# Optimization experiments

Hardware: AMD Instinct MI355X
Metric: run time of the kernel (lower is better)

Reference implementation:

```python
import jax, jax.numpy as jnp
import numpy as np

N_NODES = 50000
N_EDGES = 800000


def setup_inputs() -> dict:
    key = jax.random.key(0)
    ks = jax.random.split(key, 12)
    x = jax.random.normal(ks[0], (N_NODES, 500), dtype=jnp.float32)
    edge_src = jax.random.randint(ks[1], (N_EDGES,), 0, N_NODES, dtype=jnp.int32)
    edge_dst = jax.random.randint(ks[2], (N_EDGES,), 0, N_NODES, dtype=jnp.int32)
    edge_vals = jax.random.uniform(ks[3], (N_EDGES,), dtype=jnp.float32) * 0.1
    def w(k, fan_in, fan_out):
        s = 1.0 / np.sqrt(fan_in)
        return jax.random.uniform(k, (fan_in, fan_out), dtype=jnp.float32, minval=-s, maxval=s)
    W1 = w(ks[4], 500, 128)
    b1 = jnp.zeros((128,), jnp.float32)
    W2 = w(ks[5], 128, 64)
    b2 = jnp.zeros((64,), jnp.float32)
    W3 = w(ks[6], 64, 16)
    b3 = jnp.zeros((16,), jnp.float32)
    We = w(ks[7], 64, 64)
    be = jnp.zeros((64,), jnp.float32)
    return {"x": x, "edge_vals": edge_vals, "W1": W1, "b1": b1, "W2": W2,
            "b2": b2, "W3": W3, "b3": b3, "We": We, "be": be,
            "edge_src": edge_src, "edge_dst": edge_dst}


def reference(x, edge_vals, W1, b1, W2, b2, W3, b3, We, be, edge_src, edge_dst):
    n = x.shape[0]

    def gcn_layer(h, W, b):
        # GraphConvolution: support = h @ W ; out = spmm(adj, support) + b
        support = h @ W                                   # [N, d_out]
        msg = support[edge_dst] * edge_vals[:, None]      # [E, d_out]
        agg = jax.ops.segment_sum(msg, edge_src, num_segments=n)
        return agg + b

    h = jax.nn.relu(gcn_layer(x, W1, b1))
    # dropout omitted (eval mode, training=False)
    h = jax.nn.relu(gcn_layer(h, W2, b2))
    out1 = jax.nn.log_softmax(gcn_layer(h, W3, b3), axis=1)
    out2 = h @ We + be
    return (out1, out2)
```

## Files before the change

kernel.cpp:

```cpp
#include <hip/hip_runtime.h>
#include <hip/hip_bf16.h>
#include <math.h>

#define N_NODES 50000
#define N_EDGES 800000

typedef __attribute__((ext_vector_type(8))) short bf16x8;
typedef __attribute__((ext_vector_type(4))) float f32x4;

__device__ inline unsigned short f2bf(float f) {
    unsigned u = __float_as_uint(f);
    unsigned r = (u + 0x7fffu + ((u >> 16) & 1u)) >> 16;
    return (unsigned short)r;
}

__device__ inline bf16x8 pack8(float4 a0, float4 a1) {
    union { __hip_bfloat162 h2[4]; bf16x8 v; } u;
    u.h2[0] = __float22bfloat162_rn(make_float2(a0.x, a0.y));
    u.h2[1] = __float22bfloat162_rn(make_float2(a0.z, a0.w));
    u.h2[2] = __float22bfloat162_rn(make_float2(a1.x, a1.y));
    u.h2[3] = __float22bfloat162_rn(make_float2(a1.z, a1.w));
    return u.v;
}

__global__ __launch_bounds__(256) void convert_weights_kernel(
    const float* __restrict__ W1, const float* __restrict__ W2,
    const float* __restrict__ We, const float* __restrict__ W3,
    unsigned short* __restrict__ W1frag, unsigned short* __restrict__ W2bf,
    unsigned short* __restrict__ Wcat)
{
    int t = blockIdx.x * 256 + threadIdx.x;
    if (t < 65536) {
        int h = t >> 15;
        int r1 = t & 32767;
        int j = r1 >> 13;
        int r2 = r1 & 8191;
        int s = r2 >> 9;
        int r3 = r2 & 511;
        int lane = r3 >> 3, jj = r3 & 7;
        int k = s * 32 + (lane >> 4) * 8 + jj;
        int n = h * 64 + j * 16 + (lane & 15);
        float v = (k < 500) ? W1[k * 128 + n] : 0.0f;
        W1frag[t] = f2bf(v);
    } else if (t < 65536 + 8192) {
        int t2 = t - 65536;
        int n = t2 >> 7, k = t2 & 127;
        W2bf[t2] = f2bf(W2[k * 64 + n]);
    } else if (t < 65536 + 8192 + 5120) {
        int t3 = t - 65536 - 8192;
        int n = t3 >> 6, k = t3 & 63;
        float v = (n < 64) ? We[k * 64 + n] : W3[k * 16 + (n - 64)];
        Wcat[t3] = f2bf(v);
    }
}

__global__ __launch_bounds__(256, 2) void gemm1_mfma_kernel(
    const float* __restrict__ A,
    const unsigned short* __restrict__ W1frag,
    unsigned short* __restrict__ C)
{
    __shared__ __align__(16) unsigned short Bs[32768];

    const int t = threadIdx.x;
    const int h  = blockIdx.x & 1;
    const int br = blockIdx.x >> 1;
    const int lane = t & 63;
    const int wave = t >> 6;
    const int r = lane & 15, q = lane >> 4;

    {
        const uint4* src = reinterpret_cast<const uint4*>(W1frag + h * 32768);
        uint4* dst = reinterpret_cast<uint4*>(Bs);
#pragma unroll
        for (int i = 0; i < 16; ++i)
            dst[t + i * 256] = src[t + i * 256];
    }
    __syncthreads();

    const int col0 = h * 64;

    for (int c = br * 4 + wave; c < 3125; c += 1024) {
        const float* ap = A + (size_t)(c * 16 + r) * 500;

        f32x4 acc[4];
#pragma unroll
        for (int j = 0; j < 4; ++j) acc[j] = {0.f, 0.f, 0.f, 0.f};

#pragma unroll 4
        for (int s = 0; s < 16; ++s) {
            const int kb = s * 32 + q * 8;
            const int k0 = kb < 496 ? kb : 496;
            const int k1 = (kb + 4) < 496 ? (kb + 4) : 496;
            float4 a0 = *reinterpret_cast<const float4*>(ap + k0);
            float4 a1 = *reinterpret_cast<const float4*>(ap + k1);
            bf16x8 af = pack8(a0, a1);
#pragma unroll
            for (int j = 0; j < 4; ++j) {
                bf16x8 b = *reinterpret_cast<const bf16x8*>(
                    &Bs[(size_t)((j * 16 + s) * 64 + lane) * 8]);
                acc[j] = __builtin_amdgcn_mfma_f32_16x16x32_bf16(af, b, acc[j], 0, 0, 0);
            }
        }

#pragma unroll
        for (int reg = 0; reg < 4; ++reg) {
            const int grow = c * 16 + q * 4 + reg;
#pragma unroll
            for (int j = 0; j < 4; ++j)
                C[(size_t)grow * 128 + col0 + j * 16 + r] = f2bf(acc[j][reg]);
        }
    }
}

__global__ __launch_bounds__(256) void gemm2_mfma_kernel(
    const unsigned short* __restrict__ A,
    const unsigned short* __restrict__ Bt,
    unsigned short* __restrict__ C)
{
    const int wid  = (blockIdx.x * 256 + threadIdx.x) >> 6;
    const int lane = threadIdx.x & 63;
    const int r = lane & 15, q = lane >> 4;
    const int row0 = wid * 16;
    const int arow = row0 + r;
    const bool valid = arow < N_NODES;
    const unsigned short* ap = A + (size_t)arow * 128 + q * 8;

    const f32x4 zero = {0.0f, 0.0f, 0.0f, 0.0f};
    f32x4 acc[4];
#pragma unroll
    for (int j = 0; j < 4; ++j) acc[j] = zero;

#pragma unroll
    for (int s = 0; s < 4; ++s) {
        bf16x8 af = {};
        if (valid) af = *reinterpret_cast<const bf16x8*>(ap + s * 32);
#pragma unroll
        for (int j = 0; j < 4; ++j) {
            bf16x8 bfr = *reinterpret_cast<const bf16x8*>(
                Bt + (size_t)(j * 16 + r) * 128 + s * 32 + q * 8);
            acc[j] = __builtin_amdgcn_mfma_f32_16x16x32_bf16(af, bfr, acc[j], 0, 0, 0);
        }
    }

#pragma unroll
    for (int reg = 0; reg < 4; ++reg) {
        int grow = row0 + q * 4 + reg;
        if (grow < N_NODES) {
#pragma unroll
            for (int j = 0; j < 4; ++j)
                C[(size_t)grow * 64 + j * 16 + r] = f2bf(acc[j][reg]);
        }
    }
}

__global__ __launch_bounds__(256) void gemm3_mfma_kernel(
    const unsigned short* __restrict__ A,
    const unsigned short* __restrict__ Bt,
    const float* __restrict__ be,
    float* __restrict__ out2,
    float* __restrict__ sup3)
{
    const int wid  = (blockIdx.x * 256 + threadIdx.x) >> 6;
    const int lane = threadIdx.x & 63;
    const int r = lane & 15, q = lane >> 4;
    const int row0 = wid * 16;
    const int arow = row0 + r;
    const bool valid = arow < N_NODES;
    const unsigned short* ap = A + (size_t)arow * 64 + q * 8;

    const f32x4 zero = {0.0f, 0.0f, 0.0f, 0.0f};
    f32x4 acc[5];
#pragma unroll
    for (int j = 0; j < 5; ++j) acc[j] = zero;

#pragma unroll
    for (int s = 0; s < 2; ++s) {
        bf16x8 af = {};
        if (valid) af = *reinterpret_cast<const bf16x8*>(ap + s * 32);
#pragma unroll
        for (int j = 0; j < 5; ++j) {
            bf16x8 bfr = *reinterpret_cast<const bf16x8*>(
                Bt + (size_t)(j * 16 + r) * 64 + s * 32 + q * 8);
            acc[j] = __builtin_amdgcn_mfma_f32_16x16x32_bf16(af, bfr, acc[j], 0, 0, 0);
        }
    }

    float bev[4];
#pragma unroll
    for (int j = 0; j < 4; ++j) bev[j] = be[j * 16 + r];

#pragma unroll
    for (int reg = 0; reg < 4; ++reg) {
        int grow = row0 + q * 4 + reg;
        if (grow < N_NODES) {
#pragma unroll
            for (int j = 0; j < 4; ++j)
                out2[(size_t)grow * 64 + j * 16 + r] = acc[j][reg] + bev[j];
            sup3[(size_t)grow * 16 + r] = acc[4][reg];
        }
    }
}

__global__ __launch_bounds__(256) void hist_kernel(
    const int* __restrict__ src, int* __restrict__ counts)
{
    int e = blockIdx.x * 256 + threadIdx.x;
    if (e < N_EDGES) atomicAdd(&counts[src[e]], 1);
}

__global__ __launch_bounds__(1024) void scan_kernel(
    const int* __restrict__ counts, int* __restrict__ row_ptr,
    int* __restrict__ cursor)
{
    constexpr int Q = N_NODES / 4;
    const int t = threadIdx.x;
    const int lane = t & 63, wave = t >> 6;
    __shared__ int wsum[16];
    __shared__ int carry_s;
    int carry = 0;
    const int4* c4 = reinterpret_cast<const int4*>(counts);
    int4* rp4 = reinterpret_cast<int4*>(row_ptr);
    int4* cu4 = reinterpret_cast<int4*>(cursor);

    for (int base = 0; base < Q; base += 1024) {
        const int g = base + t;
        int4 v = {0, 0, 0, 0};
        if (g < Q) v = c4[g];
        const int s = v.x + v.y + v.z + v.w;

        int incl = s;
#pragma unroll
        for (int off = 1; off < 64; off <<= 1) {
            int n = __shfl_up(incl, off, 64);
            if (lane >= off) incl += n;
        }
        if (lane == 63) wsum[wave] = incl;
        __syncthreads();
        if (t < 16) {
            int w = wsum[t];
            int inc = w;
#pragma unroll
            for (int off = 1; off < 16; off <<= 1) {
                int n = __shfl_up(inc, off, 64);
                if (t >= off) inc += n;
            }
            wsum[t] = inc - w;
            if (t == 15) carry_s = inc;
        }
        __syncthreads();
        if (g < Q) {
            int e0 = carry + wsum[wave] + (incl - s);
            int4 r;
            r.x = e0;
            r.y = r.x + v.x;
            r.z = r.y + v.y;
            r.w = r.z + v.z;
            rp4[g] = r;
            cu4[g] = r;
        }
        carry += carry_s;
        __syncthreads();
    }
    if (t == 0) row_ptr[N_NODES] = carry;
}

__global__ __launch_bounds__(256) void fill_kernel(
    const int* __restrict__ src, const int* __restrict__ dst,
    const float* __restrict__ vals, int* __restrict__ cursor,
    int2* __restrict__ pairs)
{
    int e = blockIdx.x * 256 + threadIdx.x;
    if (e >= N_EDGES) return;
    int pos = atomicAdd(&cursor[src[e]], 1);
    pairs[pos] = make_int2(dst[e], __float_as_int(vals[e]));
}

__global__ __launch_bounds__(256) void gather128_bf16_kernel(
    const unsigned short* __restrict__ support, const int2* __restrict__ pairs,
    const int* __restrict__ row_ptr, const float* __restrict__ b1,
    unsigned short* __restrict__ h1)
{
    const int node = blockIdx.x * 16 + (threadIdx.x >> 4);
    if (node >= N_NODES) return;
    const int lane = threadIdx.x & 15;
    int i = row_ptr[node];
    const int end = row_ptr[node + 1];

    float acc[8] = {};
    for (; i + 2 <= end; i += 2) {
        int2 p0 = pairs[i], p1 = pairs[i + 1];
        float v0 = __int_as_float(p0.y), v1 = __int_as_float(p1.y);
        uint4 r0 = *reinterpret_cast<const uint4*>(
            support + (size_t)p0.x * 128 + lane * 8);
        uint4 r1 = *reinterpret_cast<const uint4*>(
            support + (size_t)p1.x * 128 + lane * 8);
        unsigned w0[4] = {r0.x, r0.y, r0.z, r0.w};
        unsigned w1[4] = {r1.x, r1.y, r1.z, r1.w};
#pragma unroll
        for (int j = 0; j < 4; ++j) {
            acc[2 * j]     += __uint_as_float(w0[j] << 16) * v0;
            acc[2 * j + 1] += __uint_as_float(w0[j] & 0xffff0000u) * v0;
            acc[2 * j]     += __uint_as_float(w1[j] << 16) * v1;
            acc[2 * j + 1] += __uint_as_float(w1[j] & 0xffff0000u) * v1;
        }
    }
    if (i < end) {
        int2 p = pairs[i];
        float v = __int_as_float(p.y);
        uint4 r = *reinterpret_cast<const uint4*>(
            support + (size_t)p.x * 128 + lane * 8);
        unsigned w[4] = {r.x, r.y, r.z, r.w};
#pragma unroll
        for (int j = 0; j < 4; ++j) {
            acc[2 * j]     += __uint_as_float(w[j] << 16) * v;
            acc[2 * j + 1] += __uint_as_float(w[j] & 0xffff0000u) * v;
        }
    }
    const float4 ba = *reinterpret_cast<const float4*>(b1 + lane * 8);
    const float4 bb = *reinterpret_cast<const float4*>(b1 + lane * 8 + 4);
    float bias[8] = {ba.x, ba.y, ba.z, ba.w, bb.x, bb.y, bb.z, bb.w};
    unsigned short h[8];
#pragma unroll
    for (int j = 0; j < 8; ++j) {
        float v = acc[j] + bias[j];
        h[j] = f2bf(v > 0.0f ? v : 0.0f);
    }
    *reinterpret_cast<uint4*>(h1 + (size_t)node * 128 + lane * 8) =
        *reinterpret_cast<uint4*>(h);
}

__global__ __launch_bounds__(256) void gather64_bf16_kernel(
    const unsigned short* __restrict__ support, const int2* __restrict__ pairs,
    const int* __restrict__ row_ptr, const float* __restrict__ b2,
    unsigned short* __restrict__ h2)
{
    const int node = blockIdx.x * 32 + (threadIdx.x >> 3);
    if (node >= N_NODES) return;
    const int lane = threadIdx.x & 7;
    int i = row_ptr[node];
    const int end = row_ptr[node + 1];

    float acc[8] = {};
    for (; i + 2 <= end; i += 2) {
        int2 p0 = pairs[i], p1 = pairs[i + 1];
        float v0 = __int_as_float(p0.y), v1 = __int_as_float(p1.y);
        uint4 r0 = *reinterpret_cast<const uint4*>(
            support + (size_t)p0.x * 64 + lane * 8);
        uint4 r1 = *reinterpret_cast<const uint4*>(
            support + (size_t)p1.x * 64 + lane * 8);
        unsigned w0[4] = {r0.x, r0.y, r0.z, r0.w};
        unsigned w1[4] = {r1.x, r1.y, r1.z, r1.w};
#pragma unroll
        for (int j = 0; j < 4; ++j) {
            acc[2 * j]     += __uint_as_float(w0[j] << 16) * v0;
            acc[2 * j + 1] += __uint_as_float(w0[j] & 0xffff0000u) * v0;
            acc[2 * j]     += __uint_as_float(w1[j] << 16) * v1;
            acc[2 * j + 1] += __uint_as_float(w1[j] & 0xffff0000u) * v1;
        }
    }
    if (i < end) {
        int2 p = pairs[i];
        float v = __int_as_float(p.y);
        uint4 r = *reinterpret_cast<const uint4*>(
            support + (size_t)p.x * 64 + lane * 8);
        unsigned w[4] = {r.x, r.y, r.z, r.w};
#pragma unroll
        for (int j = 0; j < 4; ++j) {
            acc[2 * j]     += __uint_as_float(w[j] << 16) * v;
            acc[2 * j + 1] += __uint_as_float(w[j] & 0xffff0000u) * v;
        }
    }
    const float4 ba = *reinterpret_cast<const float4*>(b2 + lane * 8);
    const float4 bb = *reinterpret_cast<const float4*>(b2 + lane * 8 + 4);
    float bias[8] = {ba.x, ba.y, ba.z, ba.w, bb.x, bb.y, bb.z, bb.w};
    unsigned short h[8];
#pragma unroll
    for (int j = 0; j < 8; ++j) {
        float v = acc[j] + bias[j];
        h[j] = f2bf(v > 0.0f ? v : 0.0f);
    }
    *reinterpret_cast<uint4*>(h2 + (size_t)node * 64 + lane * 8) =
        *reinterpret_cast<uint4*>(h);
}

__global__ __launch_bounds__(256) void gather16_kernel(
    const float* __restrict__ support, const int2* __restrict__ pairs,
    const int* __restrict__ row_ptr, float* __restrict__ agg)
{
    const int node = blockIdx.x * 64 + (threadIdx.x >> 2);
    if (node >= N_NODES) return;
    const int lane = threadIdx.x & 3;
    int i = row_ptr[node];
    const int end = row_ptr[node + 1];

    float4 acc0 = {0, 0, 0, 0};
    float4 acc1 = {0, 0, 0, 0};

    for (; i + 2 <= end; i += 2) {
        int2 p0 = pairs[i];
        int2 p1 = pairs[i + 1];
        float v0 = __int_as_float(p0.y);
        float v1 = __int_as_float(p1.y);
        const float4 m0 = *reinterpret_cast<const float4*>(
            support + (size_t)p0.x * 16 + lane * 4);
        const float4 m1 = *reinterpret_cast<const float4*>(
            support + (size_t)p1.x * 16 + lane * 4);
        acc0.x += m0.x * v0; acc0.y += m0.y * v0;
        acc0.z += m0.z * v0; acc0.w += m0.w * v0;
        acc1.x += m1.x * v1; acc1.y += m1.y * v1;
        acc1.z += m1.z * v1; acc1.w += m1.w * v1;
    }
    if (i < end) {
        int2 p = pairs[i];
        float v = __int_as_float(p.y);
        const float4 m = *reinterpret_cast<const float4*>(
            support + (size_t)p.x * 16 + lane * 4);
        acc0.x += m.x * v; acc0.y += m.y * v;
        acc0.z += m.z * v; acc0.w += m.w * v;
    }
    acc0.x += acc1.x; acc0.y += acc1.y; acc0.z += acc1.z; acc0.w += acc1.w;
    *reinterpret_cast<float4*>(agg + (size_t)node * 16 + lane * 4) = acc0;
}

__global__ __launch_bounds__(256) void logsoftmax_kernel(
    const float* __restrict__ agg, const float* __restrict__ b3,
    float* __restrict__ out)
{
    int row = blockIdx.x * 256 + threadIdx.x;
    if (row >= N_NODES) return;
    float v[16];
    const float4* p = reinterpret_cast<const float4*>(agg + (size_t)row * 16);
#pragma unroll
    for (int i = 0; i < 4; ++i) {
        float4 q = p[i];
        v[i * 4 + 0] = q.x + b3[i * 4 + 0];
        v[i * 4 + 1] = q.y + b3[i * 4 + 1];
        v[i * 4 + 2] = q.z + b3[i * 4 + 2];
        v[i * 4 + 3] = q.w + b3[i * 4 + 3];
    }
    float mx = v[0];
#pragma unroll
    for (int i = 1; i < 16; ++i) mx = fmaxf(mx, v[i]);
    float s = 0.0f;
#pragma unroll
    for (int i = 0; i < 16; ++i) s += expf(v[i] - mx);
    float lse = mx + logf(s);
    float4* o = reinterpret_cast<float4*>(out + (size_t)row * 16);
#pragma unroll
    for (int i = 0; i < 4; ++i)
        o[i] = make_float4(v[i * 4 + 0] - lse, v[i * 4 + 1] - lse,
                           v[i * 4 + 2] - lse, v[i * 4 + 3] - lse);
}

extern "C" void kernel_launch(void* const* d_in, const int* in_sizes, int n_in,
                              void* d_out, int out_size, void* d_ws, size_t ws_size,
                              hipStream_t stream)
{
    const float* x         = (const float*)d_in[0];
    const float* edge_vals = (const float*)d_in[1];
    const float* W1 = (const float*)d_in[2];
    const float* b1 = (const float*)d_in[3];
    const float* W2 = (const float*)d_in[4];
    const float* b2 = (const float*)d_in[5];
    const float* W3 = (const float*)d_in[6];
    const float* b3 = (const float*)d_in[7];
    const float* We = (const float*)d_in[8];
    const float* be = (const float*)d_in[9];
    const int* esrc = (const int*)d_in[10];
    const int* edst = (const int*)d_in[11];

    float* out1 = (float*)d_out;
    float* out2 = (float*)d_out + (size_t)N_NODES * 16;

    char* ws = (char*)d_ws;
    float* bufA    = (float*)(ws);
    float* bufB    = (float*)(ws + 25600000);
    float* bufC    = (float*)(ws + 51200000);
    int*   counts  = (int*)  (ws + 54400000);
    int*   row_ptr = (int*)  (ws + 54600064);
    int*   cursor  = (int*)  (ws + 54800128);
    int2*  pairs   = (int2*) (ws + 55000192);

    unsigned short* W1frag = (unsigned short*)bufC;
    unsigned short* W2bf = (unsigned short*)((char*)bufC + 131072);
    unsigned short* Wcat = (unsigned short*)((char*)bufC + 147456);

    unsigned short* sup1bf = (unsigned short*)bufA;
    unsigned short* h1bf   = (unsigned short*)bufB;
    unsigned short* sup2bf = (unsigned short*)bufA;
    unsigned short* h2bf   = (unsigned short*)bufB;
    float*          sup3   = bufA;
    float*          agg3   = bufC;

    const int WB = (N_NODES / 16 + 3) / 4;
    const int EB = (N_EDGES + 255) / 256;

    convert_weights_kernel<<<308, 256, 0, stream>>>(W1, W2, We, W3, W1frag, W2bf, Wcat);
    hipMemsetAsync(counts, 0, (size_t)N_NODES * 4, stream);
    hist_kernel<<<EB, 256, 0, stream>>>(esrc, counts);
    scan_kernel<<<1, 1024, 0, stream>>>(counts, row_ptr, cursor);
    fill_kernel<<<EB, 256, 0, stream>>>(esrc, edst, edge_vals, cursor, pairs);

    gemm1_mfma_kernel<<<512, 256, 0, stream>>>(x, W1frag, sup1bf);

    gather128_bf16_kernel<<<(N_NODES + 15) / 16, 256, 0, stream>>>(
        sup1bf, pairs, row_ptr, b1, h1bf);

    gemm2_mfma_kernel<<<WB, 256, 0, stream>>>(h1bf, W2bf, sup2bf);

    gather64_bf16_kernel<<<(N_NODES + 31) / 32, 256, 0, stream>>>(
        sup2bf, pairs, row_ptr, b2, h2bf);

    gemm3_mfma_kernel<<<WB, 256, 0, stream>>>(h2bf, Wcat, be, out2, sup3);

    gather16_kernel<<<(N_NODES + 63) / 64, 256, 0, stream>>>(
        sup3, pairs, row_ptr, agg3);

    logsoftmax_kernel<<<(N_NODES + 255) / 256, 256, 0, stream>>>(agg3, b3, out1);
}
```

Baseline: 371.1 us.

## Fuse weight conversion with histogram, fuse gather16 with log-softmax, widen gathers

Merges the weight-conversion and edge-histogram kernels into one launch and fuses the layer-3 gather with log-softmax, which removes the intermediate agg buffer and two launches. The gather kernels now give each node a full wavefront that splits its edges across lane groups and combines them with xor shuffles, to get more memory-level parallelism per node. The small GEMMs load pre-fragmented weights into LDS instead of reading strided global memory. Risks: more threads sit idle on low-degree nodes, and the shuffle reductions add work.

```diff
diff --git a/kernel.cpp b/kernel.cpp
--- a/kernel.cpp
+++ b/kernel.cpp
@@ -23,189 +23,49 @@
     return u.v;
 }
 
-__global__ __launch_bounds__(256) void convert_weights_kernel(
+__global__ __launch_bounds__(256) void convert_hist_kernel(
     const float* __restrict__ W1, const float* __restrict__ W2,
     const float* __restrict__ We, const float* __restrict__ W3,
-    unsigned short* __restrict__ W1frag, unsigned short* __restrict__ W2bf,
-    unsigned short* __restrict__ Wcat)
-{
-    int t = blockIdx.x * 256 + threadIdx.x;
-    if (t < 65536) {
-        int h = t >> 15;
-        int r1 = t & 32767;
-        int j = r1 >> 13;
-        int r2 = r1 & 8191;
-        int s = r2 >> 9;
-        int r3 = r2 & 511;
-        int lane = r3 >> 3, jj = r3 & 7;
-        int k = s * 32 + (lane >> 4) * 8 + jj;
-        int n = h * 64 + j * 16 + (lane & 15);
-        float v = (k < 500) ? W1[k * 128 + n] : 0.0f;
-        W1frag[t] = f2bf(v);
-    } else if (t < 65536 + 8192) {
-        int t2 = t - 65536;
-        int n = t2 >> 7, k = t2 & 127;
-        W2bf[t2] = f2bf(W2[k * 64 + n]);
-    } else if (t < 65536 + 8192 + 5120) {
-        int t3 = t - 65536 - 8192;
-        int n = t3 >> 6, k = t3 & 63;
-        float v = (n < 64) ? We[k * 64 + n] : W3[k * 16 + (n - 64)];
-        Wcat[t3] = f2bf(v);
-    }
-}
-
-__global__ __launch_bounds__(256, 2) void gemm1_mfma_kernel(
-    const float* __restrict__ A,
-    const unsigned short* __restrict__ W1frag,
-    unsigned short* __restrict__ C)
-{
-    __shared__ __align__(16) unsigned short Bs[32768];
-
-    const int t = threadIdx.x;
-    const int h  = blockIdx.x & 1;
-    const int br = blockIdx.x >> 1;
-    const int lane = t & 63;
-    const int wave = t >> 6;
-    const int r = lane & 15, q = lane >> 4;
-
-    {
-        const uint4* src = reinterpret_cast<const uint4*>(W1frag + h * 32768);
-        uint4* dst = reinterpret_cast<uint4*>(Bs);
-#pragma unroll
-        for (int i = 0; i < 16; ++i)
-            dst[t + i * 256] = src[t + i * 256];
-    }
-    __syncthreads();
-
-    const int col0 = h * 64;
-
-    for (int c = br * 4 + wave; c < 3125; c += 1024) {
-        const float* ap = A + (size_t)(c * 16 + r) * 500;
-
-        f32x4 acc[4];
-#pragma unroll
-        for (int j = 0; j < 4; ++j) acc[j] = {0.f, 0.f, 0.f, 0.f};
-
-#pragma unroll 4
-        for (int s = 0; s < 16; ++s) {
-            const int kb = s * 32 + q * 8;
-            const int k0 = kb < 496 ? kb : 496;
-            const int k1 = (kb + 4) < 496 ? (kb + 4) : 496;
-            float4 a0 = *reinterpret_cast<const float4*>(ap + k0);
-            float4 a1 = *reinterpret_cast<const float4*>(ap + k1);
-            bf16x8 af = pack8(a0, a1);
-#pragma unroll
-            for (int j = 0; j < 4; ++j) {
-                bf16x8 b = *reinterpret_cast<const bf16x8*>(
-                    &Bs[(size_t)((j * 16 + s) * 64 + lane) * 8]);
-                acc[j] = __builtin_amdgcn_mfma_f32_16x16x32_bf16(af, b, acc[j], 0, 0, 0);
-            }
-        }
-
-#pragma unroll
-        for (int reg = 0; reg < 4; ++reg) {
-            const int grow = c * 16 + q * 4 + reg;
-#pragma unroll
-            for (int j = 0; j < 4; ++j)
-                C[(size_t)grow * 128 + col0 + j * 16 + r] = f2bf(acc[j][reg]);
-        }
-    }
-}
-
-__global__ __launch_bounds__(256) void gemm2_mfma_kernel(
-    const unsigned short* __restrict__ A,
-    const unsigned short* __restrict__ Bt,
-    unsigned short* __restrict__ C)
-{
-    const int wid  = (blockIdx.x * 256 + threadIdx.x) >> 6;
-    const int lane = threadIdx.x & 63;
-    const int r = lane & 15, q = lane >> 4;
-    const int row0 = wid * 16;
-    const int arow = row0 + r;
-    const bool valid = arow < N_NODES;
-    const unsigned short* ap = A + (size_t)arow * 128 + q * 8;
-
-    const f32x4 zero = {0.0f, 0.0f, 0.0f, 0.0f};
-    f32x4 acc[4];
-#pragma unroll
-    for (int j = 0; j < 4; ++j) acc[j] = zero;
-
-#pragma unroll
-    for (int s = 0; s < 4; ++s) {
-        bf16x8 af = {};
-        if (valid) af = *reinterpret_cast<const bf16x8*>(ap + s * 32);
-#pragma unroll
-        for (int j = 0; j < 4; ++j) {
-            bf16x8 bfr = *reinterpret_cast<const bf16x8*>(
-                Bt + (size_t)(j * 16 + r) * 128 + s * 32 + q * 8);
-            acc[j] = __builtin_amdgcn_mfma_f32_16x16x32_bf16(af, bfr, acc[j], 0, 0, 0);
-        }
-    }
-
-#pragma unroll
-    for (int reg = 0; reg < 4; ++reg) {
-        int grow = row0 + q * 4 + reg;
-        if (grow < N_NODES) {
-#pragma unroll
-            for (int j = 0; j < 4; ++j)
-                C[(size_t)grow * 64 + j * 16 + r] = f2bf(acc[j][reg]);
-        }
-    }
-}
-
-__global__ __launch_bounds__(256) void gemm3_mfma_kernel(
-    const unsigned short* __restrict__ A,
-    const unsigned short* __restrict__ Bt,
-    const float* __restrict__ be,
-    float* __restrict__ out2,
-    float* __restrict__ sup3)
-{
-    const int wid  = (blockIdx.x * 256 + threadIdx.x) >> 6;
-    const int lane = threadIdx.x & 63;
-    const int r = lane & 15, q = lane >> 4;
-    const int row0 = wid * 16;
-    const int arow = row0 + r;
-    const bool valid = arow < N_NODES;
-    const unsigned short* ap = A + (size_t)arow * 64 + q * 8;
-
-    const f32x4 zero = {0.0f, 0.0f, 0.0f, 0.0f};
-    f32x4 acc[5];
-#pragma unroll
-    for (int j = 0; j < 5; ++j) acc[j] = zero;
-
-#pragma unroll
-    for (int s = 0; s < 2; ++s) {
-        bf16x8 af = {};
-        if (valid) af = *reinterpret_cast<const bf16x8*>(ap + s * 32);
-#pragma unroll
-        for (int j = 0; j < 5; ++j) {
-            bf16x8 bfr = *reinterpret_cast<const bf16x8*>(
-                Bt + (size_t)(j * 16 + r) * 64 + s * 32 + q * 8);
-            acc[j] = __builtin_amdgcn_mfma_f32_16x16x32_bf16(af, bfr, acc[j], 0, 0, 0);
-        }
-    }
-
-    float bev[4];
-#pragma unroll
-    for (int j = 0; j < 4; ++j) bev[j] = be[j * 16 + r];
-
-#pragma unroll
-    for (int reg = 0; reg < 4; ++reg) {
-        int grow = row0 + q * 4 + reg;
-        if (grow < N_NODES) {
-#pragma unroll
-            for (int j = 0; j < 4; ++j)
-                out2[(size_t)grow * 64 + j * 16 + r] = acc[j][reg] + bev[j];
-            sup3[(size_t)grow * 16 + r] = acc[4][reg];
-        }
-    }
-}
-
-__global__ __launch_bounds__(256) void hist_kernel(
+    unsigned short* __restrict__ W1frag, unsigned short* __restrict__ W2frag,
+    unsigned short* __restrict__ Wcfrag,
     const int* __restrict__ src, int* __restrict__ counts)
 {
-    int e = blockIdx.x * 256 + threadIdx.x;
-    if (e < N_EDGES) atomicAdd(&counts[src[e]], 1);
+    if (blockIdx.x < 308) {
+        int t = blockIdx.x * 256 + threadIdx.x;
+        if (t < 65536) {
+            int h = t >> 15;
+            int r1 = t & 32767;
+            int j = r1 >> 13;
+            int r2 = r1 & 8191;
+            int s = r2 >> 9;
+            int r3 = r2 & 511;
+            int lane = r3 >> 3, jj = r3 & 7;
+            int k = s * 32 + (lane >> 4) * 8 + jj;
+            int n = h * 64 + j * 16 + (lane & 15);
+            float v = (k < 500) ? W1[k * 128 + n] : 0.0f;
+            W1frag[t] = f2bf(v);
+        } else if (t < 73728) {
+            int t2 = t - 65536;
+            int j = t2 >> 11;
+            int s = (t2 >> 9) & 3;
+            int lane = (t2 >> 3) & 63, jj = t2 & 7;
+            int k = s * 32 + (lane >> 4) * 8 + jj;
+            int n = j * 16 + (lane & 15);
+            W2frag[t2] = f2bf(W2[k * 64 + n]);
+        } else {
+            int t3 = t - 73728;
+            int j = t3 >> 10;
+            int s = (t3 >> 9) & 1;
+            int lane = (t3 >> 3) & 63, jj = t3 & 7;
+            int k = s * 32 + (lane >> 4) * 8 + jj;
+            int n = j * 16 + (lane & 15);
+            float v = (n < 64) ? We[k * 64 + n] : W3[k * 16 + (n - 64)];
+            Wcfrag[t3] = f2bf(v);
+        }
+    } else {
+        int e = (blockIdx.x - 308) * 256 + threadIdx.x;
+        if (e < N_EDGES) atomicAdd(&counts[src[e]], 1);
+    }
 }
 
 __global__ __launch_bounds__(1024) void scan_kernel(
@@ -275,25 +135,185 @@
     pairs[pos] = make_int2(dst[e], __float_as_int(vals[e]));
 }
 
-__global__ __launch_bounds__(256) void gather128_bf16_kernel(
+__global__ __launch_bounds__(256, 2) void gemm1_mfma_kernel(
+    const float* __restrict__ A,
+    const unsigned short* __restrict__ W1frag,
+    unsigned short* __restrict__ C)
+{
+    __shared__ __align__(16) unsigned short Bs[32768];
+
+    const int t = threadIdx.x;
+    const int h  = blockIdx.x & 1;
+    const int br = blockIdx.x >> 1;
+    const int lane = t & 63;
+    const int wave = t >> 6;
+    const int r = lane & 15, q = lane >> 4;
+
+    {
+        const uint4* src = reinterpret_cast<const uint4*>(W1frag + h * 32768);
+        uint4* dst = reinterpret_cast<uint4*>(Bs);
+#pragma unroll
+        for (int i = 0; i < 16; ++i)
+            dst[t + i * 256] = src[t + i * 256];
+    }
+    __syncthreads();
+
+    const int col0 = h * 64;
+
+    for (int c = br * 4 + wave; c < 3125; c += 1024) {
+        const float* ap = A + (size_t)(c * 16 + r) * 500;
+
+        f32x4 acc[4];
+#pragma unroll
+        for (int j = 0; j < 4; ++j) acc[j] = {0.f, 0.f, 0.f, 0.f};
+
+#pragma unroll 4
+        for (int s = 0; s < 16; ++s) {
+            const int kb = s * 32 + q * 8;
+            const int k0 = kb < 496 ? kb : 496;
+            const int k1 = (kb + 4) < 496 ? (kb + 4) : 496;
+            float4 a0 = *reinterpret_cast<const float4*>(ap + k0);
+            float4 a1 = *reinterpret_cast<const float4*>(ap + k1);
+            bf16x8 af = pack8(a0, a1);
+#pragma unroll
+            for (int j = 0; j < 4; ++j) {
+                bf16x8 b = *reinterpret_cast<const bf16x8*>(
+                    &Bs[(size_t)((j * 16 + s) * 64 + lane) * 8]);
+                acc[j] = __builtin_amdgcn_mfma_f32_16x16x32_bf16(af, b, acc[j], 0, 0, 0);
+            }
+        }
+
+#pragma unroll
+        for (int reg = 0; reg < 4; ++reg) {
+            const int grow = c * 16 + q * 4 + reg;
+#pragma unroll
+            for (int j = 0; j < 4; ++j)
+                C[(size_t)grow * 128 + col0 + j * 16 + r] = f2bf(acc[j][reg]);
+        }
+    }
+}
+
+__global__ __launch_bounds__(256) void gemm2_mfma_kernel(
+    const unsigned short* __restrict__ A,
+    const unsigned short* __restrict__ W2frag,
+    unsigned short* __restrict__ C)
+{
+    __shared__ __align__(16) unsigned short Bs[8192];
+
+    const int t = threadIdx.x;
+    const int lane = t & 63, wave = t >> 6;
+    const int r = lane & 15, q = lane >> 4;
+
+    {
+        const uint4* src = reinterpret_cast<const uint4*>(W2frag);
+        uint4* dst = reinterpret_cast<uint4*>(Bs);
+#pragma unroll
+        for (int i = 0; i < 4; ++i)
+            dst[t + i * 256] = src[t + i * 256];
+    }
+    __syncthreads();
+
+    const int c = blockIdx.x * 4 + wave;
+    if (c >= 3125) return;
+    const unsigned short* ap = A + (size_t)(c * 16 + r) * 128 + q * 8;
+
+    f32x4 acc[4];
+#pragma unroll
+    for (int j = 0; j < 4; ++j) acc[j] = {0.f, 0.f, 0.f, 0.f};
+
+#pragma unroll
+    for (int s = 0; s < 4; ++s) {
+        bf16x8 af = *reinterpret_cast<const bf16x8*>(ap + s * 32);
+#pragma unroll
+        for (int j = 0; j < 4; ++j) {
+            bf16x8 b = *reinterpret_cast<const bf16x8*>(
+                &Bs[(size_t)((j * 4 + s) * 64 + lane) * 8]);
+            acc[j] = __builtin_amdgcn_mfma_f32_16x16x32_bf16(af, b, acc[j], 0, 0, 0);
+        }
+    }
+
+#pragma unroll
+    for (int reg = 0; reg < 4; ++reg) {
+        const int grow = c * 16 + q * 4 + reg;
+#pragma unroll
+        for (int j = 0; j < 4; ++j)
+            C[(size_t)grow * 64 + j * 16 + r] = f2bf(acc[j][reg]);
+    }
+}
+
+__global__ __launch_bounds__(256) void gemm3_mfma_kernel(
+    const unsigned short* __restrict__ A,
+    const unsigned short* __restrict__ Wcfrag,
+    const float* __restrict__ be,
+    float* __restrict__ out2,
+    float* __restrict__ sup3)
+{
+    __shared__ __align__(16) unsigned short Bs[5120];
+
+    const int t = threadIdx.x;
+    const int lane = t & 63, wave = t >> 6;
+    const int r = lane & 15, q = lane >> 4;
+
+    {
+        const uint4* src = reinterpret_cast<const uint4*>(Wcfrag);
+        uint4* dst = reinterpret_cast<uint4*>(Bs);
+#pragma unroll
+        for (int i = 0; i < 2; ++i)
+            dst[t + i * 256] = src[t + i * 256];
+        if (t < 128) dst[512 + t] = src[512 + t];
+    }
+    __syncthreads();
+
+    const int c = blockIdx.x * 4 + wave;
+    if (c >= 3125) return;
+    const unsigned short* ap = A + (size_t)(c * 16 + r) * 64 + q * 8;
+
+    f32x4 acc[5];
+#pragma unroll
+    for (int j = 0; j < 5; ++j) acc[j] = {0.f, 0.f, 0.f, 0.f};
+
+#pragma unroll
+    for (int s = 0; s < 2; ++s) {
+        bf16x8 af = *reinterpret_cast<const bf16x8*>(ap + s * 32);
+#pragma unroll
+        for (int j = 0; j < 5; ++j) {
+            bf16x8 b = *reinterpret_cast<const bf16x8*>(
+                &Bs[(size_t)((j * 2 + s) * 64 + lane) * 8]);
+            acc[j] = __builtin_amdgcn_mfma_f32_16x16x32_bf16(af, b, acc[j], 0, 0, 0);
+        }
+    }
+
+    float bev[4];
+#pragma unroll
+    for (int j = 0; j < 4; ++j) bev[j] = be[j * 16 + r];
+
+#pragma unroll
+    for (int reg = 0; reg < 4; ++reg) {
+        const int grow = c * 16 + q * 4 + reg;
+#pragma unroll
+        for (int j = 0; j < 4; ++j)
+            out2[(size_t)grow * 64 + j * 16 + r] = acc[j][reg] + bev[j];
+        sup3[(size_t)grow * 16 + r] = acc[4][reg];
+    }
+}
+
+__global__ __launch_bounds__(256) void gather128_kernel(
     const unsigned short* __restrict__ support, const int2* __restrict__ pairs,
     const int* __restrict__ row_ptr, const float* __restrict__ b1,
     unsigned short* __restrict__ h1)
 {
-    const int node = blockIdx.x * 16 + (threadIdx.x >> 4);
-    if (node >= N_NODES) return;
-    const int lane = threadIdx.x & 15;
-    int i = row_ptr[node];
+    const int node = blockIdx.x * 4 + (threadIdx.x >> 6);
+    const int lane = threadIdx.x & 63;
+    const int f = lane & 15, e = lane >> 4;
+    int i = row_ptr[node] + e;
     const int end = row_ptr[node + 1];
 
     float acc[8] = {};
-    for (; i + 2 <= end; i += 2) {
-        int2 p0 = pairs[i], p1 = pairs[i + 1];
+    for (; i + 4 < end; i += 8) {
+        int2 p0 = pairs[i], p1 = pairs[i + 4];
         float v0 = __int_as_float(p0.y), v1 = __int_as_float(p1.y);
-        uint4 r0 = *reinterpret_cast<const uint4*>(
-            support + (size_t)p0.x * 128 + lane * 8);
-        uint4 r1 = *reinterpret_cast<const uint4*>(
-            support + (size_t)p1.x * 128 + lane * 8);
+        uint4 r0 = *reinterpret_cast<const uint4*>(support + (size_t)p0.x * 128 + f * 8);
+        uint4 r1 = *reinterpret_cast<const uint4*>(support + (size_t)p1.x * 128 + f * 8);
         unsigned w0[4] = {r0.x, r0.y, r0.z, r0.w};
         unsigned w1[4] = {r1.x, r1.y, r1.z, r1.w};
 #pragma unroll
@@ -307,8 +327,7 @@
     if (i < end) {
         int2 p = pairs[i];
         float v = __int_as_float(p.y);
-        uint4 r = *reinterpret_cast<const uint4*>(
-            support + (size_t)p.x * 128 + lane * 8);
+        uint4 r = *reinterpret_cast<const uint4*>(support + (size_t)p.x * 128 + f * 8);
         unsigned w[4] = {r.x, r.y, r.z, r.w};
 #pragma unroll
         for (int j = 0; j < 4; ++j) {
@@ -316,38 +335,43 @@
             acc[2 * j + 1] += __uint_as_float(w[j] & 0xffff0000u) * v;
         }
     }
-    const float4 ba = *reinterpret_cast<const float4*>(b1 + lane * 8);
-    const float4 bb = *reinterpret_cast<const float4*>(b1 + lane * 8 + 4);
-    float bias[8] = {ba.x, ba.y, ba.z, ba.w, bb.x, bb.y, bb.z, bb.w};
-    unsigned short h[8];
 #pragma unroll
     for (int j = 0; j < 8; ++j) {
-        float v = acc[j] + bias[j];
-        h[j] = f2bf(v > 0.0f ? v : 0.0f);
-    }
-    *reinterpret_cast<uint4*>(h1 + (size_t)node * 128 + lane * 8) =
-        *reinterpret_cast<uint4*>(h);
-}
-
-__global__ __launch_bounds__(256) void gather64_bf16_kernel(
+        acc[j] += __shfl_xor(acc[j], 16, 64);
+        acc[j] += __shfl_xor(acc[j], 32, 64);
+    }
+    if (e == 0) {
+        const float4 ba = *reinterpret_cast<const float4*>(b1 + f * 8);
+        const float4 bb = *reinterpret_cast<const float4*>(b1 + f * 8 + 4);
+        float bias[8] = {ba.x, ba.y, ba.z, ba.w, bb.x, bb.y, bb.z, bb.w};
+        unsigned short h[8];
+#pragma unroll
+        for (int j = 0; j < 8; ++j) {
+            float v = acc[j] + bias[j];
+            h[j] = f2bf(v > 0.0f ? v : 0.0f);
+        }
+        *reinterpret_cast<uint4*>(h1 + (size_t)node * 128 + f * 8) =
+            *reinterpret_cast<uint4*>(h);
+    }
+}
+
+__global__ __launch_bounds__(256) void gather64_kernel(
     const unsigned short* __restrict__ support, const int2* __restrict__ pairs,
     const int* __restrict__ row_ptr, const float* __restrict__ b2,
     unsigned short* __restrict__ h2)
 {
-    const int node = blockIdx.x * 32 + (threadIdx.x >> 3);
-    if (node >= N_NODES) return;
-    const int lane = threadIdx.x & 7;
-    int i = row_ptr[node];
+    const int node = blockIdx.x * 4 + (threadIdx.x >> 6);
+    const int lane = threadIdx.x & 63;
+    const int f = lane & 7, e = lane >> 3;
+    int i = row_ptr[node] + e;
     const int end = row_ptr[node + 1];
 
     float acc[8] = {};
-    for (; i + 2 <= end; i += 2) {
-        int2 p0 = pairs[i], p1 = pairs[i + 1];
+    for (; i + 8 < end; i += 16) {
+        int2 p0 = pairs[i], p1 = pairs[i + 8];
         float v0 = __int_as_float(p0.y), v1 = __int_as_float(p1.y);
-        uint4 r0 = *reinterpret_cast<const uint4*>(
-            support + (size_t)p0.x * 64 + lane * 8);
-        uint4 r1 = *reinterpret_cast<const uint4*>(
-            support + (size_t)p1.x * 64 + lane * 8);
+        uint4 r0 = *reinterpret_cast<const uint4*>(support + (size_t)p0.x * 64 + f * 8);
+        uint4 r1 = *reinterpret_cast<const uint4*>(support + (size_t)p1.x * 64 + f * 8);
         unsigned w0[4] = {r0.x, r0.y, r0.z, r0.w};
         unsigned w1[4] = {r1.x, r1.y, r1.z, r1.w};
 #pragma unroll
@@ -361,8 +385,7 @@
     if (i < end) {
         int2 p = pairs[i];
         float v = __int_as_float(p.y);
-        uint4 r = *reinterpret_cast<const uint4*>(
-            support + (size_t)p.x * 64 + lane * 8);
+        uint4 r = *reinterpret_cast<const uint4*>(support + (size_t)p.x * 64 + f * 8);
         unsigned w[4] = {r.x, r.y, r.z, r.w};
 #pragma unroll
         for (int j = 0; j < 4; ++j) {
@@ -370,86 +393,75 @@
             acc[2 * j + 1] += __uint_as_float(w[j] & 0xffff0000u) * v;
         }
     }
-    const float4 ba = *reinterpret_cast<const float4*>(b2 + lane * 8);
-    const float4 bb = *reinterpret_cast<const float4*>(b2 + lane * 8 + 4);
-    float bias[8] = {ba.x, ba.y, ba.z, ba.w, bb.x, bb.y, bb.z, bb.w};
-    unsigned short h[8];
 #pragma unroll
     for (int j = 0; j < 8; ++j) {
-        float v = acc[j] + bias[j];
-        h[j] = f2bf(v > 0.0f ? v : 0.0f);
-    }
-    *reinterpret_cast<uint4*>(h2 + (size_t)node * 64 + lane * 8) =
-        *reinterpret_cast<uint4*>(h);
-}
-
-__global__ __launch_bounds__(256) void gather16_kernel(
-    const float* __restrict__ support, const int2* __restrict__ pairs,
-    const int* __restrict__ row_ptr, float* __restrict__ agg)
-{
-    const int node = blockIdx.x * 64 + (threadIdx.x >> 2);
-    if (node >= N_NODES) return;
-    const int lane = threadIdx.x & 3;
-    int i = row_ptr[node];
+        acc[j] += __shfl_xor(acc[j], 8, 64);
+        acc[j] += __shfl_xor(acc[j], 16, 64);
+        acc[j] += __shfl_xor(acc[j], 32, 64);
+    }
+    if (e == 0) {
+        const float4 ba = *reinterpret_cast<const float4*>(b2 + f * 8);
+        const float4 bb = *reinterpret_cast<const float4*>(b2 + f * 8 + 4);
+        float bias[8] = {ba.x, ba.y, ba.z, ba.w, bb.x, bb.y, bb.z, bb.w};
+        unsigned short h[8];
+#pragma unroll
+        for (int j = 0; j < 8; ++j) {
+            float v = acc[j] + bias[j];
+            h[j] = f2bf(v > 0.0f ? v : 0.0f);
+        }
+        *reinterpret_cast<uint4*>(h2 + (size_t)node * 64 + f * 8) =
+            *reinterpret_cast<uint4*>(h);
+    }
+}
+
+__global__ __launch_bounds__(256) void gather16_lsm_kernel(
+    const float* __restrict__ sup3, const int2* __restrict__ pairs,
+    const int* __restrict__ row_ptr, const float* __restrict__ b3,
+    float* __restrict__ out1)
+{
+    const int node = blockIdx.x * 4 + (threadIdx.x >> 6);
+    const int lane = threadIdx.x & 63;
+    const int f = lane & 3, e = lane >> 2;
+    int i = row_ptr[node] + e;
     const int end = row_ptr[node + 1];
 
-    float4 acc0 = {0, 0, 0, 0};
-    float4 acc1 = {0, 0, 0, 0};
-
-    for (; i + 2 <= end; i += 2) {
-        int2 p0 = pairs[i];
-        int2 p1 = pairs[i + 1];
-        float v0 = __int_as_float(p0.y);
-        float v1 = __int_as_float(p1.y);
-        const float4 m0 = *reinterpret_cast<const float4*>(
-            support + (size_t)p0.x * 16 + lane * 4);
-        const float4 m1 = *reinterpret_cast<const float4*>(
-            support + (size_t)p1.x * 16 + lane * 4);
-        acc0.x += m0.x * v0; acc0.y += m0.y * v0;
-        acc0.z += m0.z * v0; acc0.w += m0.w * v0;
-        acc1.x += m1.x * v1; acc1.y += m1.y * v1;
-        acc1.z += m1.z * v1; acc1.w += m1.w * v1;
+    float4 acc = {0, 0, 0, 0};
+    for (; i + 16 < end; i += 32) {
+        int2 p0 = pairs[i], p1 = pairs[i + 16];
+        float v0 = __int_as_float(p0.y), v1 = __int_as_float(p1.y);
+        float4 m0 = *reinterpret_cast<const float4*>(sup3 + (size_t)p0.x * 16 + f * 4);
+        float4 m1 = *reinterpret_cast<const float4*>(sup3 + (size_t)p1.x * 16 + f * 4);
+        acc.x += m0.x * v0 + m1.x * v1;
+        acc.y += m0.y * v0 + m1.y * v1;
+        acc.z += m0.z * v0 + m1.z * v1;
+        acc.w += m0.w * v0 + m1.w * v1;
     }
     if (i < end) {
         int2 p = pairs[i];
         float v = __int_as_float(p.y);
-        const float4 m = *reinterpret_cast<const float4*>(
-            support + (size_t)p.x * 16 + lane * 4);
-        acc0.x += m.x * v; acc0.y += m.y * v;
-        acc0.z += m.z * v; acc0.w += m.w * v;
-    }
-    acc0.x += acc1.x; acc0.y += acc1.y; acc0.z += acc1.z; acc0.w += acc1.w;
-    *reinterpret_cast<float4*>(agg + (size_t)node * 16 + lane * 4) = acc0;
-}
-
-__global__ __launch_bounds__(256) void logsoftmax_kernel(
-    const float* __restrict__ agg, const float* __restrict__ b3,
-    float* __restrict__ out)
-{
-    int row = blockIdx.x * 256 + threadIdx.x;
-    if (row >= N_NODES) return;
-    float v[16];
-    const float4* p = reinterpret_cast<const float4*>(agg + (size_t)row * 16);
-#pragma unroll
-    for (int i = 0; i < 4; ++i) {
-        float4 q = p[i];
-        v[i * 4 + 0] = q.x + b3[i * 4 + 0];
-        v[i * 4 + 1] = q.y + b3[i * 4 + 1];
-        v[i * 4 + 2] = q.z + b3[i * 4 + 2];
-        v[i * 4 + 3] = q.w + b3[i * 4 + 3];
-    }
-    float mx = v[0];
-#pragma unroll
-    for (int i = 1; i < 16; ++i) mx = fmaxf(mx, v[i]);
-    float s = 0.0f;
-#pragma unroll
-    for (int i = 0; i < 16; ++i) s += expf(v[i] - mx);
-    float lse = mx + logf(s);
-    float4* o = reinterpret_cast<float4*>(out + (size_t)row * 16);
-#pragma unroll
-    for (int i = 0; i < 4; ++i)
-        o[i] = make_float4(v[i * 4 + 0] - lse, v[i * 4 + 1] - lse,
-                           v[i * 4 + 2] - lse, v[i * 4 + 3] - lse);
+        float4 m = *reinterpret_cast<const float4*>(sup3 + (size_t)p.x * 16 + f * 4);
+        acc.x += m.x * v; acc.y += m.y * v; acc.z += m.z * v; acc.w += m.w * v;
+    }
+#pragma unroll
+    for (int off = 4; off < 64; off <<= 1) {
+        acc.x += __shfl_xor(acc.x, off, 64);
+        acc.y += __shfl_xor(acc.y, off, 64);
+        acc.z += __shfl_xor(acc.z, off, 64);
+        acc.w += __shfl_xor(acc.w, off, 64);
+    }
+    const float4 b = *reinterpret_cast<const float4*>(b3 + f * 4);
+    float a0 = acc.x + b.x, a1 = acc.y + b.y, a2 = acc.z + b.z, a3 = acc.w + b.w;
+    float mx = fmaxf(fmaxf(a0, a1), fmaxf(a2, a3));
+    mx = fmaxf(mx, __shfl_xor(mx, 1, 64));
+    mx = fmaxf(mx, __shfl_xor(mx, 2, 64));
+    float s = expf(a0 - mx) + expf(a1 - mx) + expf(a2 - mx) + expf(a3 - mx);
+    s += __shfl_xor(s, 1, 64);
+    s += __shfl_xor(s, 2, 64);
+    const float lse = mx + logf(s);
+    if (e == 0) {
+        float4 o = {a0 - lse, a1 - lse, a2 - lse, a3 - lse};
+        *reinterpret_cast<float4*>(out1 + (size_t)node * 16 + f * 4) = o;
+    }
 }
 
 extern "C" void kernel_launch(void* const* d_in, const int* in_sizes, int n_in,
@@ -482,39 +494,34 @@
     int2*  pairs   = (int2*) (ws + 55000192);
 
     unsigned short* W1frag = (unsigned short*)bufC;
-    unsigned short* W2bf = (unsigned short*)((char*)bufC + 131072);
-    unsigned short* Wcat = (unsigned short*)((char*)bufC + 147456);
+    unsigned short* W2frag = (unsigned short*)((char*)bufC + 131072);
+    unsigned short* Wcfrag = (unsigned short*)((char*)bufC + 147456);
 
     unsigned short* sup1bf = (unsigned short*)bufA;
     unsigned short* h1bf   = (unsigned short*)bufB;
     unsigned short* sup2bf = (unsigned short*)bufA;
     unsigned short* h2bf   = (unsigned short*)bufB;
     float*          sup3   = bufA;
-    float*          agg3   = bufC;
-
-    const int WB = (N_NODES / 16 + 3) / 4;
-    const int EB = (N_EDGES + 255) / 256;
-
-    convert_weights_kernel<<<308, 256, 0, stream>>>(W1, W2, We, W3, W1frag, W2bf, Wcat);
+
+    const int EB  = (N_EDGES + 255) / 256;
+    const int GN  = N_NODES / 4;
+    const int G23 = 782;
+
     hipMemsetAsync(counts, 0, (size_t)N_NODES * 4, stream);
-    hist_kernel<<<EB, 256, 0, stream>>>(esrc, counts);
+    convert_hist_kernel<<<308 + EB, 256, 0, stream>>>(
+        W1, W2, We, W3, W1frag, W2frag, Wcfrag, esrc, counts);
     scan_kernel<<<1, 1024, 0, stream>>>(counts, row_ptr, cursor);
     fill_kernel<<<EB, 256, 0, stream>>>(esrc, edst, edge_vals, cursor, pairs);
 
     gemm1_mfma_kernel<<<512, 256, 0, stream>>>(x, W1frag, sup1bf);
 
-    gather128_bf16_kernel<<<(N_NODES + 15) / 16, 256, 0, stream>>>(
-        sup1bf, pairs, row_ptr, b1, h1bf);
-
-    gemm2_mfma_kernel<<<WB, 256, 0, stream>>>(h1bf, W2bf, sup2bf);
-
-    gather64_bf16_kernel<<<(N_NODES + 31) / 32, 256, 0, stream>>>(
-        sup2bf, pairs, row_ptr, b2, h2bf);
-
-    gemm3_mfma_kernel<<<WB, 256, 0, stream>>>(h2bf, Wcat, be, out2, sup3);
-
-    gather16_kernel<<<(N_NODES + 63) / 64, 256, 0, stream>>>(
-        sup3, pairs, row_ptr, agg3);
-
-    logsoftmax_kernel<<<(N_NODES + 255) / 256, 256, 0, stream>>>(agg3, b3, out1);
-}
+    gather128_kernel<<<GN, 256, 0, stream>>>(sup1bf, pairs, row_ptr, b1, h1bf);
+
+    gemm2_mfma_kernel<<<G23, 256, 0, stream>>>(h1bf, W2frag, sup2bf);
+
+    gather64_kernel<<<GN, 256, 0, stream>>>(sup2bf, pairs, row_ptr, b2, h2bf);
+
+    gemm3_mfma_kernel<<<G23, 256, 0, stream>>>(h2bf, Wcfrag, be, out2, sup3);
+
+    gather16_lsm_kernel<<<GN, 256, 0, stream>>>(sup3, pairs, row_ptr, b3, out1);
+}
```

Measured after the change: 370.3 us. About the same (-0.2%).
